# Kernel tuning notes

Measured on AMD Instinct MI355X. Metric: run time of the kernel, lower is better.

Reference implementation:

```python
import jax, jax.numpy as jnp
import numpy as np

MAX_ITERS = 50
EPS_NORM = 1e-8
EPS_SEP = -1e-6


def setup_inputs() -> dict:
    key = jax.random.key(0)
    k1, k2 = jax.random.split(key)
    pointcloud = jax.random.normal(k1, (200000, 3), dtype=jnp.float32)
    targets = jax.random.normal(k2, (256, 3), dtype=jnp.float32)
    return {"pointcloud": pointcloud, "targets": targets}


def reference(pointcloud, targets):
    # pointcloud: [N, d], targets: [M, d]
    N = pointcloud.shape[0]
    M = targets.shape[0]
    p2 = jnp.sum(pointcloud * pointcloud, axis=1)  # [N]
    t2 = jnp.sum(targets * targets, axis=1)        # [M]

    def step(mask, _):
        # squared euclidean distances [M, N] (argmin identical to cdist argmin)
        d2 = t2[:, None] + p2[None, :] - 2.0 * (targets @ pointcloud.T)
        d2 = jnp.where(mask, d2, jnp.inf)
        closest_idx = jnp.argmin(d2, axis=1)           # [M]
        closest_points = pointcloud[closest_idx]       # [M, d]
        a = closest_points - targets
        a = a / (jnp.linalg.norm(a, axis=1, keepdims=True) + EPS_NORM)
        b = jnp.sum(a * closest_points, axis=1)        # [M]
        dot = a @ pointcloud.T - b[:, None]            # [M, N]
        separated = dot >= EPS_SEP
        mask = mask & ~separated
        return mask, (a, b)

    mask0 = jnp.ones((M, N), dtype=bool)
    _, (a_stack, b_stack) = jax.lax.scan(step, mask0, None, length=MAX_ITERS)
    return a_stack, b_stack  # [MAX_ITERS, M, d], [MAX_ITERS, M]
```

## Files before the change

### kernel.cpp

```cpp
#include <hip/hip_runtime.h>
#include <stdint.h>
#include <math.h>

#pragma clang fp contract(off)

#define BLOCK 1024
#define NW (BLOCK / 64)
#define PT 4
#define PB 4
#define MAX_ITERS 50
#define NEAR_CAP 9472
#define SOLO_CAP 2048
#define HB 4096
#define EPS_NORM 1e-8f
#define EPS_SEP (-1e-6f)
#define CMD_REFILL 1
#define CMD_EXIT 2

__global__ __launch_bounds__(BLOCK)
__attribute__((amdgpu_waves_per_eu(4, 4)))
void convex_plane_kernel(
    const float* __restrict__ pc, const float* __restrict__ tg,
    float* __restrict__ out, int N, int M, int stepsA)
{
    extern __shared__ uint32_t smem[];
    const int tid  = threadIdx.x;
    const int lane = tid & 63;
    const int wv   = tid >> 6;
    const int m    = blockIdx.x;

    float* sx     = (float*)smem;
    float* sy     = sx + NEAR_CAP;
    float* sz     = sy + NEAR_CAP;
    int*   sid    = (int*)(sz + NEAR_CAP);
    float* planes = (float*)(sid + NEAR_CAP);
    float* red_d  = planes + 52 * 4;
    float* red_x  = red_d + NW;
    float* red_y  = red_x + NW;
    float* red_z  = red_y + NW;
    int*   red_i  = (int*)(red_z + NW);
    int*   wsum   = red_i + NW;
    int*   ibc    = wsum + NW;
    float* fbc    = (float*)(ibc + 6);
    int*   cur    = (int*)(fbc + 3);
    int*   hist   = (int*)sx;
    const float4* pl4 = (const float4*)planes;

    const float tx = tg[3*m+0], ty = tg[3*m+1], tz = tg[3*m+2];
    const float t2 = tx*tx + ty*ty + tz*tz;

    float* out_a = out;
    float* out_b = out + (size_t)MAX_ITERS * (size_t)M * 3;

    if (tid < 52) {
        planes[4*tid+0] = 0.f; planes[4*tid+1] = 0.f;
        planes[4*tid+2] = 0.f; planes[4*tid+3] = INFINITY;
    }

    auto finishC = [&](float dmin, int imin, float mx, float my, float mz,
                       int mycnt) {
        #pragma unroll
        for (int off = 32; off > 0; off >>= 1) {
            float od = __shfl_down(dmin, off, 64);
            int   oi = __shfl_down(imin, off, 64);
            float ox = __shfl_down(mx, off, 64);
            float oy = __shfl_down(my, off, 64);
            float oz = __shfl_down(mz, off, 64);
            int   oc = __shfl_down(mycnt, off, 64);
            if (od < dmin || (od == dmin && oi < imin)) {
                dmin = od; imin = oi; mx = ox; my = oy; mz = oz;
            }
            mycnt += oc;
        }
        if (lane == 0) {
            red_d[wv] = dmin; red_i[wv] = imin;
            red_x[wv] = mx; red_y[wv] = my; red_z[wv] = mz; wsum[wv] = mycnt;
        }
        __syncthreads();
        if (wv == 0) {
            float bd = (lane < NW) ? red_d[lane] : INFINITY;
            int   bi = (lane < NW) ? red_i[lane] : 0;
            float bx = (lane < NW) ? red_x[lane] : 0.f;
            float by = (lane < NW) ? red_y[lane] : 0.f;
            float bz = (lane < NW) ? red_z[lane] : 0.f;
            int   c  = (lane < NW) ? wsum[lane]  : 0;
            #pragma unroll
            for (int off = 8; off > 0; off >>= 1) {
                float od = __shfl_down(bd, off, 64);
                int   oi = __shfl_down(bi, off, 64);
                float ox = __shfl_down(bx, off, 64);
                float oy = __shfl_down(by, off, 64);
                float oz = __shfl_down(bz, off, 64);
                int   oc = __shfl_down(c, off, 64);
                if (od < bd || (od == bd && oi < bi)) {
                    bd = od; bi = oi; bx = ox; by = oy; bz = oz;
                }
                c += oc;
            }
            if (lane == 0) {
                ibc[0] = bi; ibc[1] = cur[0]; ibc[4] = c;
                fbc[0] = bx; fbc[1] = by; fbc[2] = bz;
            }
        }
        __syncthreads();
    };

    auto buildNear = [&](int kplanes) {
        for (int h = tid; h < HB; h += BLOCK) hist[h] = 0;
        __syncthreads();
        for (int s = 0; s < stepsA; ++s) {
            const int ib = s * PT * BLOCK + tid;
            uint32_t live = 0;
            float px[PT], py[PT], pz[PT];
            #pragma unroll
            for (int j = 0; j < PT; ++j) {
                const int i = ib + j * BLOCK;
                if (i < N) {
                    live |= (1u << j);
                    const float* p = pc + 3 * (size_t)i;
                    px[j] = p[0]; py[j] = p[1]; pz[j] = p[2];
                }
            }
            for (int q0 = 0; q0 < kplanes && live; q0 += 4) {
                float4 a0 = pl4[q0], a1 = pl4[q0+1], a2 = pl4[q0+2], a3 = pl4[q0+3];
                #pragma unroll
                for (int j = 0; j < PT; ++j) if ((live >> j) & 1u) {
                    float d0 = a0.x*px[j] + a0.y*py[j] + a0.z*pz[j] - a0.w;
                    float d1 = a1.x*px[j] + a1.y*py[j] + a1.z*pz[j] - a1.w;
                    float d2t = a2.x*px[j] + a2.y*py[j] + a2.z*pz[j] - a2.w;
                    float d3 = a3.x*px[j] + a3.y*py[j] + a3.z*pz[j] - a3.w;
                    if (d0 >= EPS_SEP || d1 >= EPS_SEP || d2t >= EPS_SEP || d3 >= EPS_SEP)
                        live &= ~(1u << j);
                }
            }
            #pragma unroll
            for (int j = 0; j < PT; ++j) if ((live >> j) & 1u) {
                float p2 = px[j]*px[j] + py[j]*py[j] + pz[j]*pz[j];
                float tp = tx*px[j] + ty*py[j] + tz*pz[j];
                float d2 = t2 + p2 - 2.0f*tp;
                atomicAdd(&hist[(int)(__float_as_uint(d2) >> 20)], 1);
            }
        }
        __syncthreads();
        const int b0 = tid * (HB / BLOCK);
        const int h0 = hist[b0], h1 = hist[b0+1], h2 = hist[b0+2], h3 = hist[b0+3];
        const int ls = h0 + h1 + h2 + h3;
        int incl = ls;
        #pragma unroll
        for (int off = 1; off < 64; off <<= 1) {
            int o = __shfl_up(incl, off, 64);
            if (lane >= off) incl += o;
        }
        if (lane == 63) wsum[wv] = incl;
        if (tid == 0) ibc[2] = HB;
        __syncthreads();
        if (wv == 0 && lane < NW) {
            int v = wsum[lane];
            int i2 = v;
            #pragma unroll
            for (int off = 1; off < NW; off <<= 1) {
                int o = __shfl_up(i2, off, 64);
                if (lane >= off) i2 += o;
            }
            wsum[lane] = i2 - v;
        }
        __syncthreads();
        int ex = wsum[wv] + incl - ls;
        int c = ex;
        if (c <= NEAR_CAP && c + h0 > NEAR_CAP) ibc[2] = b0;
        c += h0; if (c <= NEAR_CAP && c + h1 > NEAR_CAP) ibc[2] = b0 + 1;
        c += h1; if (c <= NEAR_CAP && c + h2 > NEAR_CAP) ibc[2] = b0 + 2;
        c += h2; if (c <= NEAR_CAP && c + h3 > NEAR_CAP) ibc[2] = b0 + 3;
        if (tid == 0) cur[0] = 0;
        __syncthreads();
        const int Kthr = ibc[2];
        float dmin = INFINITY; int imin = 0;
        float mx = 0.f, my = 0.f, mz = 0.f;
        int mycnt = 0;
        for (int s = 0; s < stepsA; ++s) {
            const int ib = s * PT * BLOCK + tid;
            uint32_t live = 0;
            float px[PT], py[PT], pz[PT];
            #pragma unroll
            for (int j = 0; j < PT; ++j) {
                const int i = ib + j * BLOCK;
                if (i < N) {
                    live |= (1u << j);
                    const float* p = pc + 3 * (size_t)i;
                    px[j] = p[0]; py[j] = p[1]; pz[j] = p[2];
                }
            }
            for (int q0 = 0; q0 < kplanes && live; q0 += 4) {
                float4 a0 = pl4[q0], a1 = pl4[q0+1], a2 = pl4[q0+2], a3 = pl4[q0+3];
                #pragma unroll
                for (int j = 0; j < PT; ++j) if ((live >> j) & 1u) {
                    float d0 = a0.x*px[j] + a0.y*py[j] + a0.z*pz[j] - a0.w;
                    float d1 = a1.x*px[j] + a1.y*py[j] + a1.z*pz[j] - a1.w;
                    float d2t = a2.x*px[j] + a2.y*py[j] + a2.z*pz[j] - a2.w;
                    float d3 = a3.x*px[j] + a3.y*py[j] + a3.z*pz[j] - a3.w;
                    if (d0 >= EPS_SEP || d1 >= EPS_SEP || d2t >= EPS_SEP || d3 >= EPS_SEP)
                        live &= ~(1u << j);
                }
            }
            mycnt += (int)__popc(live);
            #pragma unroll
            for (int j = 0; j < PT; ++j) {
                bool nearkeep = false;
                float d2 = 0.f;
                if ((live >> j) & 1u) {
                    float p2 = px[j]*px[j] + py[j]*py[j] + pz[j]*pz[j];
                    float tp = tx*px[j] + ty*py[j] + tz*pz[j];
                    d2 = t2 + p2 - 2.0f*tp;
                    const int i = ib + j * BLOCK;
                    if (d2 < dmin || (d2 == dmin && i < imin)) {
                        dmin = d2; imin = i; mx = px[j]; my = py[j]; mz = pz[j];
                    }
                    nearkeep = ((int)(__float_as_uint(d2) >> 20) < Kthr);
                }
                unsigned long long bal = __ballot(nearkeep);
                if (bal) {
                    int base = 0;
                    if (lane == 0) base = atomicAdd(cur, (int)__popcll(bal));
                    base = __shfl(base, 0, 64);
                    if (nearkeep) {
                        int pos = base + (int)__popcll(bal & ((1ull << lane) - 1ull));
                        if (pos < NEAR_CAP) {
                            sx[pos] = px[j]; sy[pos] = py[j]; sz[pos] = pz[j];
                            sid[pos] = ib + j * BLOCK;
                        }
                    }
                }
            }
        }
        finishC(dmin, imin, mx, my, mz, mycnt);
    };

    auto scanN = [&](int count, float ax, float ay, float az, float b) {
        if (tid == 0) cur[0] = 0;
        __syncthreads();
        float dmin = INFINITY; int imin = 0;
        float mx = 0.f, my = 0.f, mz = 0.f;
        const int per = BLOCK * PB;
        const int bsteps = (count + per - 1) / per;
        for (int s = 0; s < bsteps; ++s) {
            float X[PB], Y[PB], Z[PB], D[PB]; int J[PB];
            uint32_t keepm = 0;
            #pragma unroll
            for (int q = 0; q < PB; ++q) {
                const int e = s * per + q * BLOCK + tid;
                if (e < count) {
                    float px = sx[e], py = sy[e], pz = sz[e];
                    X[q] = px; Y[q] = py; Z[q] = pz; J[q] = sid[e];
                    float dt = ax*px + ay*py + az*pz - b;
                    if (dt < EPS_SEP) {
                        keepm |= (1u << q);
                        float p2 = px*px + py*py + pz*pz;
                        float tp = tx*px + ty*py + tz*pz;
                        D[q] = t2 + p2 - 2.0f*tp;
                    }
                }
            }
            __syncthreads();
            int c = (int)__popc(keepm);
            int incl = c;
            #pragma unroll
            for (int off = 1; off < 64; off <<= 1) {
                int o = __shfl_up(incl, off, 64);
                if (lane >= off) incl += o;
            }
            const int excl = incl - c;
            const int tot  = __shfl(incl, 63, 64);
            int wb = 0;
            if (lane == 0) wb = atomicAdd(cur, tot);
            wb = __shfl(wb, 0, 64);
            int pos = wb + excl;
            #pragma unroll
            for (int q = 0; q < PB; ++q) if ((keepm >> q) & 1u) {
                sx[pos] = X[q]; sy[pos] = Y[q]; sz[pos] = Z[q]; sid[pos] = J[q];
                if (D[q] < dmin || (D[q] == dmin && J[q] < imin)) {
                    dmin = D[q]; imin = J[q]; mx = X[q]; my = Y[q]; mz = Z[q];
                }
                ++pos;
            }
        }
        finishC(dmin, imin, mx, my, mz, 0);
    };

    buildNear(0);
    int   ncount = ibc[1];
    float ccx = fbc[0], ccy = fbc[1], ccz = fbc[2];
    int k = 0;

    for (;;) {
        if (ncount == 0) {
            buildNear(k);
            ncount = ibc[1];
            ccx = fbc[0]; ccy = fbc[1]; ccz = fbc[2];
            if (ibc[4] == 0) {
                const float c0 = pc[0], c1 = pc[1], c2 = pc[2];
                const float vx = c0 - tx, vy = c1 - ty, vz = c2 - tz;
                const float nrm = sqrtf(vx*vx + vy*vy + vz*vz);
                const float den = nrm + EPS_NORM;
                const float ax = vx / den, ay = vy / den, az = vz / den;
                const float b  = ax*c0 + ay*c1 + az*c2;
                for (int q = tid; q < MAX_ITERS - k; q += BLOCK) {
                    const int kk = k + q;
                    const size_t oa = ((size_t)kk * M + m) * 3;
                    out_a[oa+0] = ax; out_a[oa+1] = ay; out_a[oa+2] = az;
                    out_b[(size_t)kk * M + m] = b;
                }
                return;
            }
        }
        if (ncount > 0 && ncount <= SOLO_CAP) break;
        const float vx = ccx - tx, vy = ccy - ty, vz = ccz - tz;
        const float nrm = sqrtf(vx*vx + vy*vy + vz*vz);
        const float den = nrm + EPS_NORM;
        const float ax = vx / den, ay = vy / den, az = vz / den;
        const float b  = ax*ccx + ay*ccy + az*ccz;
        if (tid == 0) {
            const size_t oa = ((size_t)k * M + m) * 3;
            out_a[oa+0] = ax; out_a[oa+1] = ay; out_a[oa+2] = az;
            out_b[(size_t)k * M + m] = b;
            planes[4*k+0] = ax; planes[4*k+1] = ay;
            planes[4*k+2] = az; planes[4*k+3] = b;
        }
        ++k;
        if (k == MAX_ITERS) return;
        if (ncount > 0) {
            scanN(ncount, ax, ay, az, b);
            ncount = ibc[1];
            ccx = fbc[0]; ccy = fbc[1]; ccz = fbc[2];
        }
    }

    if (wv != 0) {
        for (;;) {
            __syncthreads();
            const int c = ibc[3];
            if (c == CMD_EXIT) return;
            buildNear(ibc[5]);
        }
    }
    int scount = ncount;
    for (;;) {
        if (scount == 0) {
            if (lane == 0) { ibc[3] = CMD_REFILL; ibc[5] = k; }
            __syncthreads();
            buildNear(k);
            scount = ibc[1];
            ccx = fbc[0]; ccy = fbc[1]; ccz = fbc[2];
            if (ibc[4] == 0) {
                if (lane == 0) ibc[3] = CMD_EXIT;
                __syncthreads();
                const float c0 = pc[0], c1 = pc[1], c2 = pc[2];
                const float vx = c0 - tx, vy = c1 - ty, vz = c2 - tz;
                const float nrm = sqrtf(vx*vx + vy*vy + vz*vz);
                const float den = nrm + EPS_NORM;
                const float ax = vx / den, ay = vy / den, az = vz / den;
                const float b  = ax*c0 + ay*c1 + az*c2;
                for (int q = lane; q < MAX_ITERS - k; q += 64) {
                    const int kk = k + q;
                    const size_t oa = ((size_t)kk * M + m) * 3;
                    out_a[oa+0] = ax; out_a[oa+1] = ay; out_a[oa+2] = az;
                    out_b[(size_t)kk * M + m] = b;
                }
                return;
            }
        }
        const float vx = ccx - tx, vy = ccy - ty, vz = ccz - tz;
        const float nrm = sqrtf(vx*vx + vy*vy + vz*vz);
        const float den = nrm + EPS_NORM;
        const float ax = vx / den, ay = vy / den, az = vz / den;
        const float b  = ax*ccx + ay*ccy + az*ccz;
        if (lane == 0) {
            const size_t oa = ((size_t)k * M + m) * 3;
            out_a[oa+0] = ax; out_a[oa+1] = ay; out_a[oa+2] = az;
            out_b[(size_t)k * M + m] = b;
            planes[4*k+0] = ax; planes[4*k+1] = ay;
            planes[4*k+2] = az; planes[4*k+3] = b;
        }
        ++k;
        if (k == MAX_ITERS) {
            if (lane == 0) ibc[3] = CMD_EXIT;
            __syncthreads();
            return;
        }
        if (scount > 0) {
            float dmin = INFINITY; int imin = 0;
            float mx = 0.f, my = 0.f, mz = 0.f;
            int wcur = 0;
            const int old = scount;
            for (int g0 = 0; g0 < old; g0 += 256) {
                float X[4], Y[4], Z[4], D[4]; int J[4];
                uint32_t km = 0;
                #pragma unroll
                for (int u = 0; u < 4; ++u) {
                    const int e = g0 + u * 64 + lane;
                    if (e < old) {
                        X[u] = sx[e]; Y[u] = sy[e]; Z[u] = sz[e]; J[u] = sid[e];
                        float dt = ax*X[u] + ay*Y[u] + az*Z[u] - b;
                        if (dt < EPS_SEP) {
                            km |= (1u << u);
                            float p2 = X[u]*X[u] + Y[u]*Y[u] + Z[u]*Z[u];
                            float tp = tx*X[u] + ty*Y[u] + tz*Z[u];
                            D[u] = t2 + p2 - 2.0f*tp;
                        }
                    }
                }
                #pragma unroll
                for (int u = 0; u < 4; ++u) {
                    unsigned long long bal = __ballot(((km >> u) & 1u) != 0u);
                    int pos = wcur + (int)__popcll(bal & ((1ull << lane) - 1ull));
                    if ((km >> u) & 1u) {
                        sx[pos] = X[u]; sy[pos] = Y[u]; sz[pos] = Z[u]; sid[pos] = J[u];
                        if (D[u] < dmin || (D[u] == dmin && J[u] < imin)) {
                            dmin = D[u]; imin = J[u]; mx = X[u]; my = Y[u]; mz = Z[u];
                        }
                    }
                    wcur += (int)__popcll(bal);
                }
            }
            #pragma unroll
            for (int off = 32; off > 0; off >>= 1) {
                float od = __shfl_down(dmin, off, 64);
                int   oi = __shfl_down(imin, off, 64);
                float ox = __shfl_down(mx, off, 64);
                float oy = __shfl_down(my, off, 64);
                float oz = __shfl_down(mz, off, 64);
                if (od < dmin || (od == dmin && oi < imin)) {
                    dmin = od; imin = oi; mx = ox; my = oy; mz = oz;
                }
            }
            ccx = __shfl(mx, 0, 64);
            ccy = __shfl(my, 0, 64);
            ccz = __shfl(mz, 0, 64);
            scount = wcur;
        }
    }
}

extern "C" void kernel_launch(void* const* d_in, const int* in_sizes, int n_in,
                              void* d_out, int out_size, void* d_ws, size_t ws_size,
                              hipStream_t stream) {
    const float* pc = (const float*)d_in[0];
    const float* tg = (const float*)d_in[1];
    float* out = (float*)d_out;
    const int N = in_sizes[0] / 3;
    const int M = in_sizes[1] / 3;
    const int stepsA = (N + BLOCK * PT - 1) / (BLOCK * PT);

    const size_t words = (size_t)4 * NEAR_CAP
                       + 52 * 4
                       + 4 * NW + NW + NW
                       + 6 + 3 + 1;
    const size_t smem = words * 4;
    hipFuncSetAttribute((const void*)convex_plane_kernel,
                        hipFuncAttributeMaxDynamicSharedMemorySize, (int)smem);
    convex_plane_kernel<<<M, BLOCK, smem, stream>>>(pc, tg, out, N, M, stepsA);
}
```

Measured before the change: 596.1 us.

## Add global distance-bucketed index walk for refills and finer histogram

Raises the distance histogram from 4096 to 32768 bins and, in the first full pass, scatters the indices of points just beyond the near-set threshold into a per-target workspace array sorted by distance bucket. Later refills walk these bucketed candidates in order instead of rescanning all points, and fall back to a full scan whose points are filtered by a key floor so already-consumed buckets are skipped. This is meant to avoid repeated full passes over the point cloud when the near set runs dry. In exchange it adds global-memory atomics and scatter writes in the first pass, a larger histogram to clear and scan, and more complex control flow that depends on how much workspace is available.

```diff
diff --git a/kernel.cpp b/kernel.cpp
--- a/kernel.cpp
+++ b/kernel.cpp
@@ -11,17 +11,25 @@
 #define MAX_ITERS 50
 #define NEAR_CAP 9472
 #define SOLO_CAP 2048
-#define HB 4096
+#define HB 32768
+#define HSH 17
+#define BPT (HB / BLOCK)
+#define WARR_MAX 32768
+#define WALK_TGT 2048
 #define EPS_NORM 1e-8f
 #define EPS_SEP (-1e-6f)
 #define CMD_REFILL 1
 #define CMD_EXIT 2
+#define ST_ALIVE 0
+#define ST_DEAD 1
+#define ST_DONE 2
 
 __global__ __launch_bounds__(BLOCK)
 __attribute__((amdgpu_waves_per_eu(4, 4)))
 void convex_plane_kernel(
     const float* __restrict__ pc, const float* __restrict__ tg,
-    float* __restrict__ out, int N, int M, int stepsA)
+    float* __restrict__ out, int N, int M, int stepsA,
+    int* __restrict__ wsAll, int WARR)
 {
     extern __shared__ uint32_t smem[];
     const int tid  = threadIdx.x;
@@ -41,10 +49,13 @@
     int*   red_i  = (int*)(red_z + NW);
     int*   wsum   = red_i + NW;
     int*   ibc    = wsum + NW;
-    float* fbc    = (float*)(ibc + 6);
+    float* fbc    = (float*)(ibc + 12);
     int*   cur    = (int*)(fbc + 3);
     int*   hist   = (int*)sx;
     const float4* pl4 = (const float4*)planes;
+
+    int* ofsW = wsAll + (size_t)m * (size_t)(HB + WARR);
+    int* idxW = ofsW + HB;
 
     const float tx = tg[3*m+0], ty = tg[3*m+1], tz = tg[3*m+2];
     const float t2 = tx*tx + ty*ty + tz*tz;
@@ -105,13 +116,15 @@
         __syncthreads();
     };
 
-    auto buildNear = [&](int kplanes) {
+    auto buildNear = [&](int kplanes, int keyFloor, bool writePrefix,
+                         int capLimit) {
         for (int h = tid; h < HB; h += BLOCK) hist[h] = 0;
         __syncthreads();
         for (int s = 0; s < stepsA; ++s) {
             const int ib = s * PT * BLOCK + tid;
             uint32_t live = 0;
             float px[PT], py[PT], pz[PT];
+            int keyv[PT];
             #pragma unroll
             for (int j = 0; j < PT; ++j) {
                 const int i = ib + j * BLOCK;
@@ -120,6 +133,14 @@
                     const float* p = pc + 3 * (size_t)i;
                     px[j] = p[0]; py[j] = p[1]; pz[j] = p[2];
                 }
+            }
+            #pragma unroll
+            for (int j = 0; j < PT; ++j) if ((live >> j) & 1u) {
+                float p2 = px[j]*px[j] + py[j]*py[j] + pz[j]*pz[j];
+                float tp = tx*px[j] + ty*py[j] + tz*pz[j];
+                float d2 = t2 + p2 - 2.0f*tp;
+                keyv[j] = (int)(__float_as_uint(d2) >> HSH);
+                if (keyv[j] < keyFloor) live &= ~(1u << j);
             }
             for (int q0 = 0; q0 < kplanes && live; q0 += 4) {
                 float4 a0 = pl4[q0], a1 = pl4[q0+1], a2 = pl4[q0+2], a3 = pl4[q0+3];
@@ -134,17 +155,13 @@
                 }
             }
             #pragma unroll
-            for (int j = 0; j < PT; ++j) if ((live >> j) & 1u) {
-                float p2 = px[j]*px[j] + py[j]*py[j] + pz[j]*pz[j];
-                float tp = tx*px[j] + ty*py[j] + tz*pz[j];
-                float d2 = t2 + p2 - 2.0f*tp;
-                atomicAdd(&hist[(int)(__float_as_uint(d2) >> 20)], 1);
-            }
-        }
-        __syncthreads();
-        const int b0 = tid * (HB / BLOCK);
-        const int h0 = hist[b0], h1 = hist[b0+1], h2 = hist[b0+2], h3 = hist[b0+3];
-        const int ls = h0 + h1 + h2 + h3;
+            for (int j = 0; j < PT; ++j) if ((live >> j) & 1u)
+                atomicAdd(&hist[keyv[j]], 1);
+        }
+        __syncthreads();
+        const int b0 = tid * BPT;
+        int ls = 0;
+        for (int u = 0; u < BPT; ++u) ls += hist[b0 + u];
         int incl = ls;
         #pragma unroll
         for (int off = 1; off < 64; off <<= 1) {
@@ -152,7 +169,7 @@
             if (lane >= off) incl += o;
         }
         if (lane == 63) wsum[wv] = incl;
-        if (tid == 0) ibc[2] = HB;
+        if (tid == 0) { ibc[2] = HB; if (writePrefix) ibc[8] = HB; }
         __syncthreads();
         if (wv == 0 && lane < NW) {
             int v = wsum[lane];
@@ -165,22 +182,50 @@
             wsum[lane] = i2 - v;
         }
         __syncthreads();
-        int ex = wsum[wv] + incl - ls;
-        int c = ex;
-        if (c <= NEAR_CAP && c + h0 > NEAR_CAP) ibc[2] = b0;
-        c += h0; if (c <= NEAR_CAP && c + h1 > NEAR_CAP) ibc[2] = b0 + 1;
-        c += h1; if (c <= NEAR_CAP && c + h2 > NEAR_CAP) ibc[2] = b0 + 2;
-        c += h2; if (c <= NEAR_CAP && c + h3 > NEAR_CAP) ibc[2] = b0 + 3;
+        const int ex = wsum[wv] + incl - ls;
+        if (tid == BLOCK - 1) ibc[4] = ex + ls;
+        {
+            int c = ex;
+            for (int u = 0; u < BPT; ++u) {
+                const int hv = hist[b0 + u];
+                if (c <= capLimit && c + hv > capLimit) {
+                    ibc[2] = b0 + u;
+                    if (writePrefix) ibc[9] = c;
+                }
+                c += hv;
+            }
+        }
+        __syncthreads();
+        if (writePrefix) {
+            if (tid == 0 && ibc[2] == HB) ibc[9] = ibc[4];
+            __syncthreads();
+            const int T2 = ibc[9] + WARR;
+            int c = ex;
+            for (int u = 0; u < BPT; ++u) {
+                const int hv = hist[b0 + u];
+                if (c <= T2 && c + hv > T2) ibc[8] = b0 + u;
+                ofsW[b0 + u] = c;
+                c += hv;
+            }
+            __syncthreads();
+        }
+        const int Kthr   = ibc[2];
+        const int KB0w   = writePrefix ? ibc[8] : HB;
+        const int base0w = writePrefix ? ibc[9] : 0;
         if (tid == 0) cur[0] = 0;
         __syncthreads();
-        const int Kthr = ibc[2];
+        if (ibc[4] == 0) {
+            if (tid == 0) ibc[1] = 0;
+            __syncthreads();
+            return;
+        }
         float dmin = INFINITY; int imin = 0;
         float mx = 0.f, my = 0.f, mz = 0.f;
         int mycnt = 0;
         for (int s = 0; s < stepsA; ++s) {
             const int ib = s * PT * BLOCK + tid;
             uint32_t live = 0;
-            float px[PT], py[PT], pz[PT];
+            float px[PT], py[PT], pz[PT], d2v[PT];
             #pragma unroll
             for (int j = 0; j < PT; ++j) {
                 const int i = ib + j * BLOCK;
@@ -189,6 +234,14 @@
                     const float* p = pc + 3 * (size_t)i;
                     px[j] = p[0]; py[j] = p[1]; pz[j] = p[2];
                 }
+            }
+            #pragma unroll
+            for (int j = 0; j < PT; ++j) if ((live >> j) & 1u) {
+                float p2 = px[j]*px[j] + py[j]*py[j] + pz[j]*pz[j];
+                float tp = tx*px[j] + ty*py[j] + tz*pz[j];
+                d2v[j] = t2 + p2 - 2.0f*tp;
+                if ((int)(__float_as_uint(d2v[j]) >> HSH) < keyFloor)
+                    live &= ~(1u << j);
             }
             for (int q0 = 0; q0 < kplanes && live; q0 += 4) {
                 float4 a0 = pl4[q0], a1 = pl4[q0+1], a2 = pl4[q0+2], a3 = pl4[q0+3];
@@ -206,16 +259,18 @@
             #pragma unroll
             for (int j = 0; j < PT; ++j) {
                 bool nearkeep = false;
-                float d2 = 0.f;
                 if ((live >> j) & 1u) {
-                    float p2 = px[j]*px[j] + py[j]*py[j] + pz[j]*pz[j];
-                    float tp = tx*px[j] + ty*py[j] + tz*pz[j];
-                    d2 = t2 + p2 - 2.0f*tp;
                     const int i = ib + j * BLOCK;
-                    if (d2 < dmin || (d2 == dmin && i < imin)) {
-                        dmin = d2; imin = i; mx = px[j]; my = py[j]; mz = pz[j];
-                    }
-                    nearkeep = ((int)(__float_as_uint(d2) >> 20) < Kthr);
+                    const float d2j = d2v[j];
+                    if (d2j < dmin || (d2j == dmin && i < imin)) {
+                        dmin = d2j; imin = i; mx = px[j]; my = py[j]; mz = pz[j];
+                    }
+                    const int keyj = (int)(__float_as_uint(d2j) >> HSH);
+                    nearkeep = (keyj < Kthr);
+                    if (writePrefix && !nearkeep && keyj < KB0w) {
+                        int pos = atomicAdd(&ofsW[keyj], 1) - base0w;
+                        idxW[pos] = i;
+                    }
                 }
                 unsigned long long bal = __ballot(nearkeep);
                 if (bal) {
@@ -224,10 +279,8 @@
                     base = __shfl(base, 0, 64);
                     if (nearkeep) {
                         int pos = base + (int)__popcll(bal & ((1ull << lane) - 1ull));
-                        if (pos < NEAR_CAP) {
-                            sx[pos] = px[j]; sy[pos] = py[j]; sz[pos] = pz[j];
-                            sid[pos] = ib + j * BLOCK;
-                        }
+                        sx[pos] = px[j]; sy[pos] = py[j]; sz[pos] = pz[j];
+                        sid[pos] = ib + j * BLOCK;
                     }
                 }
             }
@@ -286,16 +339,84 @@
         finishC(dmin, imin, mx, my, mz, 0);
     };
 
-    buildNear(0);
-    int   ncount = ibc[1];
-    float ccx = fbc[0], ccy = fbc[1], ccz = fbc[2];
-    int k = 0;
-
-    for (;;) {
-        if (ncount == 0) {
-            buildNear(k);
-            ncount = ibc[1];
-            ccx = fbc[0]; ccy = fbc[1]; ccz = fbc[2];
+    auto refillAll = [&](int capLimit) -> int {
+        int k = ibc[5];
+        if (WARR > 0 && ibc[6] < ibc[8]) {
+            int wm = ibc[6];
+            const int KB0 = ibc[8], base0 = ibc[9], KNI = ibc[10];
+            if (tid == 0) cur[0] = 0;
+            __syncthreads();
+            float dmin = INFINITY; int imin = 0;
+            float mx = 0.f, my = 0.f, mz = 0.f;
+            int curNow = 0;
+            bool needFall = false;
+            while (wm < KB0) {
+                int we = ((wm >> 6) + 1) << 6;
+                if (we > KB0) we = KB0;
+                const int s0 = (wm == KNI) ? base0 : ofsW[wm - 1];
+                const int s1 = ofsW[we - 1];
+                const int cnt = s1 - s0;
+                if (curNow + cnt > NEAR_CAP) {
+                    if (curNow == 0) needFall = true;
+                    break;
+                }
+                for (int e0 = s0; e0 < s1; e0 += BLOCK) {
+                    const int e = e0 + tid;
+                    bool alive = false; int j = 0;
+                    float X = 0.f, Y = 0.f, Z = 0.f, D = 0.f;
+                    if (e < s1) {
+                        j = idxW[e - base0];
+                        const float* p = pc + 3 * (size_t)j;
+                        X = p[0]; Y = p[1]; Z = p[2];
+                        alive = true;
+                        for (int q0 = 0; q0 < k && alive; q0 += 4) {
+                            float4 a0 = pl4[q0], a1 = pl4[q0+1];
+                            float4 a2 = pl4[q0+2], a3 = pl4[q0+3];
+                            float d0 = a0.x*X + a0.y*Y + a0.z*Z - a0.w;
+                            float d1 = a1.x*X + a1.y*Y + a1.z*Z - a1.w;
+                            float d2t = a2.x*X + a2.y*Y + a2.z*Z - a2.w;
+                            float d3 = a3.x*X + a3.y*Y + a3.z*Z - a3.w;
+                            if (d0 >= EPS_SEP || d1 >= EPS_SEP ||
+                                d2t >= EPS_SEP || d3 >= EPS_SEP) alive = false;
+                        }
+                        if (alive) {
+                            float p2 = X*X + Y*Y + Z*Z;
+                            float tp = tx*X + ty*Y + tz*Z;
+                            D = t2 + p2 - 2.0f*tp;
+                        }
+                    }
+                    unsigned long long bal = __ballot(alive);
+                    if (bal) {
+                        int base = 0;
+                        if (lane == 0) base = atomicAdd(cur, (int)__popcll(bal));
+                        base = __shfl(base, 0, 64);
+                        if (alive) {
+                            int pos = base + (int)__popcll(bal & ((1ull << lane) - 1ull));
+                            sx[pos] = X; sy[pos] = Y; sz[pos] = Z; sid[pos] = j;
+                            if (D < dmin || (D == dmin && j < imin)) {
+                                dmin = D; imin = j; mx = X; my = Y; mz = Z;
+                            }
+                        }
+                    }
+                }
+                wm = we;
+                if (cnt > 0) {
+                    __syncthreads();
+                    curNow = cur[0];
+                    if (curNow >= WALK_TGT) break;
+                }
+            }
+            if (tid == 0) ibc[6] = wm;
+            if (!needFall) {
+                finishC(dmin, imin, mx, my, mz, 0);
+                if (ibc[1] > 0) return ST_ALIVE;
+            } else {
+                __syncthreads();
+            }
+        }
+        for (;;) {
+            const int fl = (WARR > 0) ? ibc[6] : ibc[6];
+            buildNear(k, fl, false, capLimit);
             if (ibc[4] == 0) {
                 const float c0 = pc[0], c1 = pc[1], c2 = pc[2];
                 const float vx = c0 - tx, vy = c1 - ty, vz = c2 - tz;
@@ -309,10 +430,55 @@
                     out_a[oa+0] = ax; out_a[oa+1] = ay; out_a[oa+2] = az;
                     out_b[(size_t)kk * M + m] = b;
                 }
-                return;
-            }
-        }
-        if (ncount > 0 && ncount <= SOLO_CAP) break;
+                return ST_DEAD;
+            }
+            if (ibc[1] > 0) {
+                if (tid == 0) ibc[6] = ibc[2];
+                __syncthreads();
+                return ST_ALIVE;
+            }
+            const float ccx = fbc[0], ccy = fbc[1], ccz = fbc[2];
+            const float vx = ccx - tx, vy = ccy - ty, vz = ccz - tz;
+            const float nrm = sqrtf(vx*vx + vy*vy + vz*vz);
+            const float den = nrm + EPS_NORM;
+            const float ax = vx / den, ay = vy / den, az = vz / den;
+            const float b  = ax*ccx + ay*ccy + az*ccz;
+            if (tid == 0) {
+                const size_t oa = ((size_t)k * M + m) * 3;
+                out_a[oa+0] = ax; out_a[oa+1] = ay; out_a[oa+2] = az;
+                out_b[(size_t)k * M + m] = b;
+                planes[4*k+0] = ax; planes[4*k+1] = ay;
+                planes[4*k+2] = az; planes[4*k+3] = b;
+            }
+            ++k;
+            if (tid == 0) ibc[5] = k;
+            if (k == MAX_ITERS) { __syncthreads(); return ST_DONE; }
+        }
+    };
+
+    buildNear(0, 0, WARR > 0, NEAR_CAP);
+    if (tid == 0) {
+        ibc[10] = ibc[2];
+        ibc[6]  = ibc[2];
+        if (WARR == 0) { ibc[8] = ibc[2]; ibc[9] = 0; }
+        ibc[5] = 0;
+        ibc[3] = 0;
+    }
+    __syncthreads();
+    int ncount = ibc[1];
+    float ccx = fbc[0], ccy = fbc[1], ccz = fbc[2];
+    int k = 0;
+
+    for (;;) {
+        if (ncount == 0) {
+            if (tid == 0) ibc[5] = k;
+            __syncthreads();
+            int st = refillAll(NEAR_CAP);
+            if (st != ST_ALIVE) return;
+            k = ibc[5]; ncount = ibc[1];
+            ccx = fbc[0]; ccy = fbc[1]; ccz = fbc[2];
+        }
+        if (ncount <= SOLO_CAP) break;
         const float vx = ccx - tx, vy = ccy - ty, vz = ccz - tz;
         const float nrm = sqrtf(vx*vx + vy*vy + vz*vz);
         const float den = nrm + EPS_NORM;
@@ -327,11 +493,9 @@
         }
         ++k;
         if (k == MAX_ITERS) return;
-        if (ncount > 0) {
-            scanN(ncount, ax, ay, az, b);
-            ncount = ibc[1];
-            ccx = fbc[0]; ccy = fbc[1]; ccz = fbc[2];
-        }
+        scanN(ncount, ax, ay, az, b);
+        ncount = ibc[1];
+        ccx = fbc[0]; ccy = fbc[1]; ccz = fbc[2];
     }
 
     if (wv != 0) {
@@ -339,7 +503,7 @@
             __syncthreads();
             const int c = ibc[3];
             if (c == CMD_EXIT) return;
-            buildNear(ibc[5]);
+            refillAll(SOLO_CAP);
         }
     }
     int scount = ncount;
@@ -347,26 +511,14 @@
         if (scount == 0) {
             if (lane == 0) { ibc[3] = CMD_REFILL; ibc[5] = k; }
             __syncthreads();
-            buildNear(k);
-            scount = ibc[1];
-            ccx = fbc[0]; ccy = fbc[1]; ccz = fbc[2];
-            if (ibc[4] == 0) {
+            int st = refillAll(SOLO_CAP);
+            if (st != ST_ALIVE) {
                 if (lane == 0) ibc[3] = CMD_EXIT;
                 __syncthreads();
-                const float c0 = pc[0], c1 = pc[1], c2 = pc[2];
-                const float vx = c0 - tx, vy = c1 - ty, vz = c2 - tz;
-                const float nrm = sqrtf(vx*vx + vy*vy + vz*vz);
-                const float den = nrm + EPS_NORM;
-                const float ax = vx / den, ay = vy / den, az = vz / den;
-                const float b  = ax*c0 + ay*c1 + az*c2;
-                for (int q = lane; q < MAX_ITERS - k; q += 64) {
-                    const int kk = k + q;
-                    const size_t oa = ((size_t)kk * M + m) * 3;
-                    out_a[oa+0] = ax; out_a[oa+1] = ay; out_a[oa+2] = az;
-                    out_b[(size_t)kk * M + m] = b;
-                }
                 return;
             }
+            k = ibc[5]; scount = ibc[1];
+            ccx = fbc[0]; ccy = fbc[1]; ccz = fbc[2];
         }
         const float vx = ccx - tx, vy = ccy - ty, vz = ccz - tz;
         const float nrm = sqrtf(vx*vx + vy*vy + vz*vz);
@@ -386,7 +538,7 @@
             __syncthreads();
             return;
         }
-        if (scount > 0) {
+        {
             float dmin = INFINITY; int imin = 0;
             float mx = 0.f, my = 0.f, mz = 0.f;
             int wcur = 0;
@@ -450,12 +602,18 @@
     const int M = in_sizes[1] / 3;
     const int stepsA = (N + BLOCK * PT - 1) / (BLOCK * PT);
 
+    long availPerBlock = (long)(ws_size / 4 / (size_t)(M > 0 ? M : 1)) - HB;
+    int WARR = 0;
+    if (availPerBlock >= 4096)
+        WARR = (int)(availPerBlock < WARR_MAX ? availPerBlock : WARR_MAX);
+
     const size_t words = (size_t)4 * NEAR_CAP
                        + 52 * 4
                        + 4 * NW + NW + NW
-                       + 6 + 3 + 1;
+                       + 12 + 3 + 1;
     const size_t smem = words * 4;
     hipFuncSetAttribute((const void*)convex_plane_kernel,
                         hipFuncAttributeMaxDynamicSharedMemorySize, (int)smem);
-    convex_plane_kernel<<<M, BLOCK, smem, stream>>>(pc, tg, out, N, M, stepsA);
+    convex_plane_kernel<<<M, BLOCK, smem, stream>>>(pc, tg, out, N, M, stepsA,
+                                                    (int*)d_ws, WARR);
 }
```

Measured after the change: 2.219 ms. 3.72x slower.
